# Kernel optimization log

Measured on AMD Instinct MI355X. Metric: run time of the kernel, lower is better.

## Reference

```python
import jax, jax.numpy as jnp
import numpy as np

B, N, IN_DIM, HID = 16, 2048, 128, 128
EPS = 1e-5


def _layer(x, W, b, g, beta):
    # x: (B, N, d_in) -> (B, N, HID)
    h = jnp.einsum('bnd,dh->bnh', x, W) + b
    mu = jnp.mean(h, axis=-1, keepdims=True)
    var = jnp.mean((h - mu) ** 2, axis=-1, keepdims=True)
    h = (h - mu) * jax.lax.rsqrt(var + EPS) * g + beta
    return jax.nn.relu(h)


def setup_inputs() -> dict:
    key = jax.random.key(0)
    ks = jax.random.split(key, 8)
    x = jax.random.normal(ks[0], (B, N, IN_DIM), dtype=jnp.float32)
    adj = jax.random.uniform(ks[1], (B, N, N), dtype=jnp.float32)
    inp = {'x': x, 'adj': adj}
    dims = [IN_DIM, HID, HID]
    for i in range(3):
        d_in = dims[i]
        scale = 1.0 / np.sqrt(d_in)
        inp[f'W{i}'] = jax.random.uniform(ks[2 + i], (d_in, HID), dtype=jnp.float32, minval=-scale, maxval=scale)
        inp[f'b{i}'] = jax.random.uniform(ks[5 + i], (HID,), dtype=jnp.float32, minval=-scale, maxval=scale)
        inp[f'g{i}'] = jnp.ones((HID,), dtype=jnp.float32)
        inp[f'be{i}'] = jnp.zeros((HID,), dtype=jnp.float32)
    return inp


def reference(x, adj, W0, b0, g0, be0, W1, b1, g1, be1, W2, b2, g2, be2):
    params = [(W0, b0, g0, be0), (W1, b1, g1, be1), (W2, b2, g2, be2)]
    h = x
    for (W, b, g, beta) in params:
        h_agg = jnp.einsum('bnm,bmd->bnd', adj, h)  # dense adjacency aggregation
        h = _layer(h_agg, W, b, g, beta)
    return h
```

## Files before the change

kernel.cpp:

```cpp
#include <hip/hip_runtime.h>
#include <hip/hip_bf16.h>

typedef __bf16 bf16;
typedef __bf16 bf16x8 __attribute__((ext_vector_type(8)));
typedef float  f32x4  __attribute__((ext_vector_type(4)));

static constexpr int NB  = 16;
static constexpr int NN  = 2048;
static constexpr int HID = 128;

__device__ __forceinline__ void gload_lds16(const bf16* g, bf16* l) {
    __builtin_amdgcn_global_load_lds(
        (const __attribute__((address_space(1))) unsigned int*)g,
        (__attribute__((address_space(3))) unsigned int*)l, 16, 0, 0);
}

#define WAITV(n) asm volatile("s_waitcnt vmcnt(" #n ")" ::: "memory")


__global__ __launch_bounds__(256) void prep_wt(const float* __restrict__ W0,
                                               const float* __restrict__ W1,
                                               const float* __restrict__ W2,
                                               bf16* __restrict__ WTg) {
    int l = blockIdx.x;
    const float* W = (l == 0) ? W0 : (l == 1) ? W1 : W2;
    bf16* out = WTg + l * 16384;
    int tid = threadIdx.x;
#pragma unroll
    for (int i = 0; i < 8; ++i) {
        int p = i * 256 + tid;
        int n = p >> 4, half = (p >> 3) & 1, cs = p & 7;
        int kc = cs ^ (n & 7);
        int kbase = half * 64 + kc * 8;
        bf16x8 o;
#pragma unroll
        for (int r = 0; r < 8; ++r) o[r] = (bf16)W[(kbase + r) * 128 + n];
        *(bf16x8*)(out + p * 8) = o;
    }
}

__global__ __launch_bounds__(256) void prep_xt(const float* __restrict__ x,
                                               bf16* __restrict__ xTt) {
    __shared__ bf16 T[128 * 136];
    const int blk = blockIdx.x;
    const int b = blk >> 4, node0 = (blk & 15) * 128;
    const int tid = threadIdx.x;
    const float* xb = x + ((size_t)b * NN + node0) * HID;
#pragma unroll
    for (int i = 0; i < 64; ++i) {
        int idx = i * 256 + tid;
        int node = idx >> 7, hid = idx & 127;
        T[hid * 136 + node] = (bf16)xb[(size_t)node * HID + hid];
    }
    __syncthreads();
#pragma unroll
    for (int i = 0; i < 8; ++i) {
        int p = i * 256 + tid;
        int half = p >> 10, p1 = p & 1023;
        int n = p1 >> 3, cs = p1 & 7, c = cs ^ (n & 7), m = half * 64 + c * 8;
        *(bf16x8*)(xTt + ((size_t)b * 32 + (node0 >> 6) + half) * 8192 + p1 * 8)
            = *(const bf16x8*)(T + n * 136 + m);
    }
}

template<int AMODE, bool FINAL>
__global__ __launch_bounds__(512, 2) void fused_layer(
        const float* __restrict__ Af, bf16* __restrict__ adjT,
        const bf16* __restrict__ Bt, const bf16* __restrict__ WTg,
        const float* __restrict__ bias, const float* __restrict__ gam,
        const float* __restrict__ bet, bf16* __restrict__ hOut,
        float* __restrict__ outF) {
    __shared__ __align__(16) bf16 lds[65536];

    const int tid = threadIdx.x, wave = tid >> 6, lane = tid & 63;
    const int c0 = lane & 15, q = lane >> 4;
    const int blk = blockIdx.x, xcd = blk & 7, jj = blk >> 3;
    const int b = xcd * 2 + (jj & 1);
    const int mtile = jj >> 1, m0 = mtile * 128;
    const int wm = wave >> 1, wn = wave & 1;

    const bf16* Btb = Bt + (size_t)b * 32 * 8192;
    bf16* Atl = adjT + ((size_t)b * 16 + mtile) * (size_t)32 * 8192;

    f32x4 acc[2][4] = {};

    auto stageA2 = [&](int buf, int kk) {
#pragma unroll
        for (int j = 0; j < 2; ++j) {
            int cb = j * 512 + wave * 64;
            gload_lds16(Atl + (size_t)kk * 8192 + (size_t)(cb + lane) * 8,
                        lds + buf * 16384 + cb * 8);
        }
    };
    auto stageB2 = [&](int buf, int kk) {
#pragma unroll
        for (int j = 0; j < 2; ++j) {
            int cb = j * 512 + wave * 64;
            gload_lds16(Btb + (size_t)kk * 8192 + (size_t)(cb + lane) * 8,
                        lds + buf * 16384 + 8192 + cb * 8);
        }
    };
    auto compute = [&](int buf) {
        const bf16* As = lds + buf * 16384;
        const bf16* Bs = As + 8192;
#pragma unroll
        for (int ks = 0; ks < 2; ++ks) {
            bf16x8 af[2], bf_[4];
#pragma unroll
            for (int mt = 0; mt < 2; ++mt) {
                int row = wm * 32 + mt * 16 + c0;
                int cb = (ks * 4 + q) ^ (row & 7);
                af[mt] = *(const bf16x8*)(As + row * 64 + cb * 8);
            }
#pragma unroll
            for (int nt = 0; nt < 4; ++nt) {
                int row = wn * 64 + nt * 16 + c0;
                int cb = (ks * 4 + q) ^ (row & 7);
                bf_[nt] = *(const bf16x8*)(Bs + row * 64 + cb * 8);
            }
            __builtin_amdgcn_s_setprio(1);
#pragma unroll
            for (int mt = 0; mt < 2; ++mt)
#pragma unroll
                for (int nt = 0; nt < 4; ++nt)
                    acc[mt][nt] = __builtin_amdgcn_mfma_f32_16x16x32_bf16(
                        af[mt], bf_[nt], acc[mt][nt], 0, 0, 0);
            __builtin_amdgcn_s_setprio(0);
        }
    };

    if constexpr (AMODE == 1) {
        int grow[2], gcb[2];
#pragma unroll
        for (int j = 0; j < 2; ++j) {
            int gi = j * 512 + tid;
            grow[j] = gi >> 3; gcb[j] = gi & 7;
        }
        f32x4 va[2], vb[2];
        auto loadA = [&](int kk) {
#pragma unroll
            for (int j = 0; j < 2; ++j) {
                const float* s = Af + (size_t)b * NN * NN
                               + (size_t)(m0 + grow[j]) * NN + kk * 64 + gcb[j] * 8;
                va[j] = *(const f32x4*)s;
                vb[j] = *(const f32x4*)(s + 4);
            }
        };
        auto writeA = [&](int buf, int kk) {
#pragma unroll
            for (int j = 0; j < 2; ++j) {
                bf16x8 o = {(bf16)va[j].x, (bf16)va[j].y, (bf16)va[j].z, (bf16)va[j].w,
                            (bf16)vb[j].x, (bf16)vb[j].y, (bf16)vb[j].z, (bf16)vb[j].w};
                int ch = grow[j] * 8 + (gcb[j] ^ (grow[j] & 7));
                *(bf16x8*)(lds + buf * 16384 + ch * 8) = o;
                *(bf16x8*)(Atl + (size_t)kk * 8192 + ch * 8) = o;
            }
        };
        loadA(0); stageB2(0, 0); writeA(0, 0);
        __syncthreads();
        int cur = 0;
        for (int kk = 0; kk < 32; ++kk) {
            if (kk < 31) { loadA(kk + 1); stageB2(cur ^ 1, kk + 1); }
            compute(cur);
            if (kk < 31) writeA(cur ^ 1, kk + 1);
            __syncthreads();
            cur ^= 1;
        }
    } else {
        stageA2(0, 0); stageB2(0, 0);
        stageA2(1, 1); stageB2(1, 1);
        stageA2(2, 2); stageB2(2, 2);
#pragma unroll 1
        for (int kk = 0; kk < 32; ++kk) {
            if (kk <= 29)      WAITV(8);
            else if (kk == 30) WAITV(4);
            else               WAITV(0);
            __builtin_amdgcn_s_barrier();
            asm volatile("" ::: "memory");
            compute(kk & 3);
            asm volatile("" ::: "memory");
            if (kk <= 28) { stageA2((kk + 3) & 3, kk + 3); stageB2((kk + 3) & 3, kk + 3); }
        }
        __syncthreads();
    }

    bf16* G = lds;
#pragma unroll
    for (int mt = 0; mt < 2; ++mt)
#pragma unroll
        for (int r = 0; r < 4; ++r) {
            int row = wm * 32 + mt * 16 + q * 4 + r;
#pragma unroll
            for (int nt = 0; nt < 4; ++nt) {
                int col = wn * 64 + nt * 16 + c0;
                G[row * 136 + col] = (bf16)acc[mt][nt][r];
            }
        }
    __syncthreads();

    f32x4 a2[8] = {};
    {
        const int gr = wave * 16 + c0;
#pragma unroll
        for (int ks = 0; ks < 4; ++ks) {
            bf16x8 af = *(const bf16x8*)(G + gr * 136 + ks * 32 + q * 8);
#pragma unroll
            for (int nt = 0; nt < 8; ++nt) {
                int n = nt * 16 + c0;
                int ch = n * 16 + (ks >> 1) * 8 + ((((ks & 1) << 2) | q) ^ (n & 7));
                bf16x8 bw = *(const bf16x8*)(WTg + (size_t)ch * 8);
                a2[nt] = __builtin_amdgcn_mfma_f32_16x16x32_bf16(af, bw, a2[nt], 0, 0, 0);
            }
        }
    }

    float bv[8], gv[8], ev[8];
#pragma unroll
    for (int nt = 0; nt < 8; ++nt) {
        int n = nt * 16 + c0;
        bv[nt] = bias[n]; gv[nt] = gam[n]; ev[nt] = bet[n];
    }
    bf16* Cs = lds;
    if constexpr (!FINAL) __syncthreads();
#pragma unroll
    for (int r = 0; r < 4; ++r) {
        float v[8], s1 = 0.f, s2 = 0.f;
#pragma unroll
        for (int nt = 0; nt < 8; ++nt) {
            float xv = a2[nt][r] + bv[nt];
            v[nt] = xv; s1 += xv; s2 += xv * xv;
        }
#pragma unroll
        for (int off = 1; off < 16; off <<= 1) {
            s1 += __shfl_xor(s1, off);
            s2 += __shfl_xor(s2, off);
        }
        float mu = s1 * (1.f / 128.f);
        float var = s2 * (1.f / 128.f) - mu * mu;
        float rs = rsqrtf(var + 1e-5f);
        int row = wave * 16 + q * 4 + r;
        if constexpr (FINAL) {
            size_t ro = ((size_t)b * NN + m0 + row) * HID;
#pragma unroll
            for (int nt = 0; nt < 8; ++nt) {
                float o = fmaxf((v[nt] - mu) * rs * gv[nt] + ev[nt], 0.f);
                outF[ro + nt * 16 + c0] = o;
            }
        } else {
#pragma unroll
            for (int nt = 0; nt < 8; ++nt) {
                float o = fmaxf((v[nt] - mu) * rs * gv[nt] + ev[nt], 0.f);
                Cs[(nt * 16 + c0) * 136 + row] = (bf16)o;
            }
        }
    }
    if constexpr (!FINAL) {
        __syncthreads();
#pragma unroll
        for (int i = 0; i < 4; ++i) {
            int p = i * 512 + tid;
            int half = p >> 10, p1 = p & 1023;
            int n = p1 >> 3, cs = p1 & 7, c = cs ^ (n & 7), m = half * 64 + c * 8;
            *(bf16x8*)(hOut + ((size_t)b * 32 + mtile * 2 + half) * 8192 + p1 * 8)
                = *(const bf16x8*)(Cs + n * 136 + m);
        }
    }
}

extern "C" void kernel_launch(void* const* d_in, const int* in_sizes, int n_in,
                              void* d_out, int out_size, void* d_ws, size_t ws_size,
                              hipStream_t stream) {
    const float* x   = (const float*)d_in[0];
    const float* adj = (const float*)d_in[1];
    const float* W[3]  = {(const float*)d_in[2],  (const float*)d_in[6],  (const float*)d_in[10]};
    const float* bb[3] = {(const float*)d_in[3],  (const float*)d_in[7],  (const float*)d_in[11]};
    const float* gg[3] = {(const float*)d_in[4],  (const float*)d_in[8],  (const float*)d_in[12]};
    const float* be[3] = {(const float*)d_in[5],  (const float*)d_in[9],  (const float*)d_in[13]};

    char* ws = (char*)d_ws;
    size_t off = 0;
    auto alloc = [&](size_t bytes) {
        char* p = ws + off; off = (off + bytes + 255) & ~(size_t)255; return p;
    };
    bf16* WTg  = (bf16*)alloc((size_t)3 * 16384 * 2);
    bf16* xTt  = (bf16*)alloc((size_t)NB * 32 * 8192 * 2);
    bf16* hT0  = (bf16*)alloc((size_t)NB * 32 * 8192 * 2);
    bf16* hT1  = (bf16*)alloc((size_t)NB * 32 * 8192 * 2);
    bf16* adjT = (bf16*)alloc((size_t)NB * 16 * 32 * 8192 * 2);

    float* outF = (float*)d_out;

    prep_wt<<<3, 256, 0, stream>>>(W[0], W[1], W[2], WTg);
    prep_xt<<<256, 256, 0, stream>>>(x, xTt);

    fused_layer<1, false><<<256, 512, 0, stream>>>(adj, adjT, xTt, WTg,
                                                   bb[0], gg[0], be[0], hT0, nullptr);
    fused_layer<2, false><<<256, 512, 0, stream>>>(adj, adjT, hT0, WTg + 16384,
                                                   bb[1], gg[1], be[1], hT1, nullptr);
    fused_layer<2, true ><<<256, 512, 0, stream>>>(adj, adjT, hT1, WTg + 2 * 16384,
                                                   bb[2], gg[2], be[2], nullptr, outF);
}
```

Before: 503.6 us.

## Split layer kernels: preload W into LDS for layer0, interleave prefetch in later layers

Splits the templated fused layer into a dedicated layer0 kernel and a layer8p kernel for the bf16-adjacency layers. Layer0 now loads the transposed weight matrix into a separate LDS region at kernel start, drops setprio, and shrinks its LDS footprint. Layer8p breaks each k-step's global-to-LDS prefetch into halves interleaved with MFMA sub-steps, separated by extra barriers, and lowers the occupancy hint to one block per CU. The goal is to spread memory issue across compute and overlap it better with MFMA, at the cost of more barriers and possibly lower occupancy.

```diff
diff --git a/kernel.cpp b/kernel.cpp
--- a/kernel.cpp
+++ b/kernel.cpp
@@ -63,14 +63,13 @@
     }
 }
 
-template<int AMODE, bool FINAL>
-__global__ __launch_bounds__(512, 2) void fused_layer(
+__global__ __launch_bounds__(512, 2) void layer0(
         const float* __restrict__ Af, bf16* __restrict__ adjT,
         const bf16* __restrict__ Bt, const bf16* __restrict__ WTg,
         const float* __restrict__ bias, const float* __restrict__ gam,
-        const float* __restrict__ bet, bf16* __restrict__ hOut,
-        float* __restrict__ outF) {
-    __shared__ __align__(16) bf16 lds[65536];
+        const float* __restrict__ bet, bf16* __restrict__ hOut) {
+    __shared__ __align__(16) bf16 lds[49152];
+    bf16* WTl = lds + 32768;
 
     const int tid = threadIdx.x, wave = tid >> 6, lane = tid & 63;
     const int c0 = lane & 15, q = lane >> 4;
@@ -84,14 +83,12 @@
 
     f32x4 acc[2][4] = {};
 
-    auto stageA2 = [&](int buf, int kk) {
-#pragma unroll
-        for (int j = 0; j < 2; ++j) {
-            int cb = j * 512 + wave * 64;
-            gload_lds16(Atl + (size_t)kk * 8192 + (size_t)(cb + lane) * 8,
-                        lds + buf * 16384 + cb * 8);
-        }
-    };
+#pragma unroll
+    for (int j = 0; j < 4; ++j) {
+        int cb = j * 512 + wave * 64;
+        gload_lds16(WTg + (size_t)(cb + lane) * 8, WTl + cb * 8);
+    }
+
     auto stageB2 = [&](int buf, int kk) {
 #pragma unroll
         for (int j = 0; j < 2; ++j) {
@@ -118,71 +115,207 @@
                 int cb = (ks * 4 + q) ^ (row & 7);
                 bf_[nt] = *(const bf16x8*)(Bs + row * 64 + cb * 8);
             }
-            __builtin_amdgcn_s_setprio(1);
 #pragma unroll
             for (int mt = 0; mt < 2; ++mt)
 #pragma unroll
                 for (int nt = 0; nt < 4; ++nt)
                     acc[mt][nt] = __builtin_amdgcn_mfma_f32_16x16x32_bf16(
                         af[mt], bf_[nt], acc[mt][nt], 0, 0, 0);
-            __builtin_amdgcn_s_setprio(0);
-        }
-    };
-
-    if constexpr (AMODE == 1) {
-        int grow[2], gcb[2];
+        }
+    };
+
+    int grow[2], gcb[2];
+#pragma unroll
+    for (int j = 0; j < 2; ++j) {
+        int gi = j * 512 + tid;
+        grow[j] = gi >> 3; gcb[j] = gi & 7;
+    }
+    f32x4 va[2], vb[2];
+    auto loadA = [&](int kk) {
 #pragma unroll
         for (int j = 0; j < 2; ++j) {
-            int gi = j * 512 + tid;
-            grow[j] = gi >> 3; gcb[j] = gi & 7;
-        }
-        f32x4 va[2], vb[2];
-        auto loadA = [&](int kk) {
-#pragma unroll
-            for (int j = 0; j < 2; ++j) {
-                const float* s = Af + (size_t)b * NN * NN
-                               + (size_t)(m0 + grow[j]) * NN + kk * 64 + gcb[j] * 8;
-                va[j] = *(const f32x4*)s;
-                vb[j] = *(const f32x4*)(s + 4);
-            }
-        };
-        auto writeA = [&](int buf, int kk) {
-#pragma unroll
-            for (int j = 0; j < 2; ++j) {
-                bf16x8 o = {(bf16)va[j].x, (bf16)va[j].y, (bf16)va[j].z, (bf16)va[j].w,
-                            (bf16)vb[j].x, (bf16)vb[j].y, (bf16)vb[j].z, (bf16)vb[j].w};
-                int ch = grow[j] * 8 + (gcb[j] ^ (grow[j] & 7));
-                *(bf16x8*)(lds + buf * 16384 + ch * 8) = o;
-                *(bf16x8*)(Atl + (size_t)kk * 8192 + ch * 8) = o;
-            }
-        };
-        loadA(0); stageB2(0, 0); writeA(0, 0);
+            const float* s = Af + (size_t)b * NN * NN
+                           + (size_t)(m0 + grow[j]) * NN + kk * 64 + gcb[j] * 8;
+            va[j] = *(const f32x4*)s;
+            vb[j] = *(const f32x4*)(s + 4);
+        }
+    };
+    auto writeA = [&](int buf, int kk) {
+#pragma unroll
+        for (int j = 0; j < 2; ++j) {
+            bf16x8 o = {(bf16)va[j].x, (bf16)va[j].y, (bf16)va[j].z, (bf16)va[j].w,
+                        (bf16)vb[j].x, (bf16)vb[j].y, (bf16)vb[j].z, (bf16)vb[j].w};
+            int ch = grow[j] * 8 + (gcb[j] ^ (grow[j] & 7));
+            *(bf16x8*)(lds + buf * 16384 + ch * 8) = o;
+            *(bf16x8*)(Atl + (size_t)kk * 8192 + ch * 8) = o;
+        }
+    };
+    loadA(0); stageB2(0, 0); writeA(0, 0);
+    __syncthreads();
+    int cur = 0;
+    for (int kk = 0; kk < 32; ++kk) {
+        if (kk < 31) { loadA(kk + 1); stageB2(cur ^ 1, kk + 1); }
+        compute(cur);
+        if (kk < 31) writeA(cur ^ 1, kk + 1);
         __syncthreads();
-        int cur = 0;
-        for (int kk = 0; kk < 32; ++kk) {
-            if (kk < 31) { loadA(kk + 1); stageB2(cur ^ 1, kk + 1); }
-            compute(cur);
-            if (kk < 31) writeA(cur ^ 1, kk + 1);
-            __syncthreads();
-            cur ^= 1;
-        }
-    } else {
-        stageA2(0, 0); stageB2(0, 0);
-        stageA2(1, 1); stageB2(1, 1);
-        stageA2(2, 2); stageB2(2, 2);
+        cur ^= 1;
+    }
+
+    bf16* G = lds;
+#pragma unroll
+    for (int mt = 0; mt < 2; ++mt)
+#pragma unroll
+        for (int r = 0; r < 4; ++r) {
+            int row = wm * 32 + mt * 16 + q * 4 + r;
+#pragma unroll
+            for (int nt = 0; nt < 4; ++nt) {
+                int col = wn * 64 + nt * 16 + c0;
+                G[row * 136 + col] = (bf16)acc[mt][nt][r];
+            }
+        }
+    __syncthreads();
+
+    f32x4 a2[8] = {};
+    {
+        const int gr = wave * 16 + c0;
+#pragma unroll
+        for (int ks = 0; ks < 4; ++ks) {
+            bf16x8 af = *(const bf16x8*)(G + gr * 136 + ks * 32 + q * 8);
+#pragma unroll
+            for (int nt = 0; nt < 8; ++nt) {
+                int n = nt * 16 + c0;
+                int ch = n * 16 + (ks >> 1) * 8 + ((((ks & 1) << 2) | q) ^ (n & 7));
+                bf16x8 bw = *(const bf16x8*)(WTl + ch * 8);
+                a2[nt] = __builtin_amdgcn_mfma_f32_16x16x32_bf16(af, bw, a2[nt], 0, 0, 0);
+            }
+        }
+    }
+
+    float bv[8], gv[8], ev[8];
+#pragma unroll
+    for (int nt = 0; nt < 8; ++nt) {
+        int n = nt * 16 + c0;
+        bv[nt] = bias[n]; gv[nt] = gam[n]; ev[nt] = bet[n];
+    }
+    bf16* Cs = lds;
+    __syncthreads();
+#pragma unroll
+    for (int r = 0; r < 4; ++r) {
+        float v[8], s1 = 0.f, s2 = 0.f;
+#pragma unroll
+        for (int nt = 0; nt < 8; ++nt) {
+            float xv = a2[nt][r] + bv[nt];
+            v[nt] = xv; s1 += xv; s2 += xv * xv;
+        }
+#pragma unroll
+        for (int off = 1; off < 16; off <<= 1) {
+            s1 += __shfl_xor(s1, off);
+            s2 += __shfl_xor(s2, off);
+        }
+        float mu = s1 * (1.f / 128.f);
+        float var = s2 * (1.f / 128.f) - mu * mu;
+        float rs = rsqrtf(var + 1e-5f);
+        int row = wave * 16 + q * 4 + r;
+#pragma unroll
+        for (int nt = 0; nt < 8; ++nt) {
+            float o = fmaxf((v[nt] - mu) * rs * gv[nt] + ev[nt], 0.f);
+            Cs[(nt * 16 + c0) * 136 + row] = (bf16)o;
+        }
+    }
+    __syncthreads();
+#pragma unroll
+    for (int i = 0; i < 4; ++i) {
+        int p = i * 512 + tid;
+        int half = p >> 10, p1 = p & 1023;
+        int n = p1 >> 3, cs = p1 & 7, c = cs ^ (n & 7), m = half * 64 + c * 8;
+        *(bf16x8*)(hOut + ((size_t)b * 32 + mtile * 2 + half) * 8192 + p1 * 8)
+            = *(const bf16x8*)(Cs + n * 136 + m);
+    }
+}
+
+template<bool FINAL>
+__global__ __launch_bounds__(512, 1) void layer8p(
+        bf16* __restrict__ adjT, const bf16* __restrict__ Bt,
+        const bf16* __restrict__ WTg,
+        const float* __restrict__ bias, const float* __restrict__ gam,
+        const float* __restrict__ bet, bf16* __restrict__ hOut,
+        float* __restrict__ outF) {
+    __shared__ __align__(16) bf16 lds[65536];
+
+    const int tid = threadIdx.x, wave = tid >> 6, lane = tid & 63;
+    const int c0 = lane & 15, q = lane >> 4;
+    const int blk = blockIdx.x, xcd = blk & 7, jj = blk >> 3;
+    const int b = xcd * 2 + (jj & 1);
+    const int mtile = jj >> 1, m0 = mtile * 128;
+    const int wm = wave >> 1, wn = wave & 1;
+
+    const bf16* Btb = Bt + (size_t)b * 32 * 8192;
+    bf16* Atl = adjT + ((size_t)b * 16 + mtile) * (size_t)32 * 8192;
+
+    f32x4 acc[2][4] = {};
+
+    auto gA = [&](int p, int kk, int buf) {
+        int cb = p * 512 + wave * 64;
+        gload_lds16(Atl + (size_t)kk * 8192 + (size_t)(cb + lane) * 8,
+                    lds + buf * 16384 + cb * 8);
+    };
+    auto gB = [&](int p, int kk, int buf) {
+        int cb = p * 512 + wave * 64;
+        gload_lds16(Btb + (size_t)kk * 8192 + (size_t)(cb + lane) * 8,
+                    lds + buf * 16384 + 8192 + cb * 8);
+    };
+
+#pragma unroll
+    for (int t = 0; t < 3; ++t) { gA(0, t, t); gA(1, t, t); gB(0, t, t); gB(1, t, t); }
+
 #pragma unroll 1
-        for (int kk = 0; kk < 32; ++kk) {
-            if (kk <= 29)      WAITV(8);
-            else if (kk == 30) WAITV(4);
-            else               WAITV(0);
-            __builtin_amdgcn_s_barrier();
-            asm volatile("" ::: "memory");
-            compute(kk & 3);
-            asm volatile("" ::: "memory");
-            if (kk <= 28) { stageA2((kk + 3) & 3, kk + 3); stageB2((kk + 3) & 3, kk + 3); }
-        }
-        __syncthreads();
-    }
+    for (int kk = 0; kk < 32; ++kk) {
+        const int buf = kk & 3, nb = (kk + 3) & 3;
+        const bool pf = (kk < 29);
+        if (kk <= 29)      WAITV(8);
+        else if (kk == 30) WAITV(4);
+        else               WAITV(0);
+        __builtin_amdgcn_s_barrier();
+        asm volatile("" ::: "memory");
+        const bf16* As = lds + buf * 16384;
+        const bf16* Bs = As + 8192;
+#pragma unroll
+        for (int ks = 0; ks < 2; ++ks) {
+            bf16x8 af[2];
+#pragma unroll
+            for (int mt = 0; mt < 2; ++mt) {
+                int row = wm * 32 + mt * 16 + c0;
+                int cb = (ks * 4 + q) ^ (row & 7);
+                af[mt] = *(const bf16x8*)(As + row * 64 + cb * 8);
+            }
+#pragma unroll
+            for (int half = 0; half < 2; ++half) {
+                if (pf) {
+                    if (ks == 0) gA(half, kk + 3, nb);
+                    else         gB(half, kk + 3, nb);
+                }
+                __builtin_amdgcn_s_barrier();
+                bf16x8 bf_[2];
+#pragma unroll
+                for (int j = 0; j < 2; ++j) {
+                    int nt = half * 2 + j;
+                    int row = wn * 64 + nt * 16 + c0;
+                    int cb = (ks * 4 + q) ^ (row & 7);
+                    bf_[j] = *(const bf16x8*)(Bs + row * 64 + cb * 8);
+                }
+                __builtin_amdgcn_s_setprio(1);
+#pragma unroll
+                for (int mt = 0; mt < 2; ++mt)
+#pragma unroll
+                    for (int j = 0; j < 2; ++j)
+                        acc[mt][half * 2 + j] = __builtin_amdgcn_mfma_f32_16x16x32_bf16(
+                            af[mt], bf_[j], acc[mt][half * 2 + j], 0, 0, 0);
+                __builtin_amdgcn_s_setprio(0);
+            }
+        }
+        asm volatile("" ::: "memory");
+    }
+    __syncthreads();
 
     bf16* G = lds;
 #pragma unroll
@@ -293,10 +426,10 @@
     prep_wt<<<3, 256, 0, stream>>>(W[0], W[1], W[2], WTg);
     prep_xt<<<256, 256, 0, stream>>>(x, xTt);
 
-    fused_layer<1, false><<<256, 512, 0, stream>>>(adj, adjT, xTt, WTg,
-                                                   bb[0], gg[0], be[0], hT0, nullptr);
-    fused_layer<2, false><<<256, 512, 0, stream>>>(adj, adjT, hT0, WTg + 16384,
-                                                   bb[1], gg[1], be[1], hT1, nullptr);
-    fused_layer<2, true ><<<256, 512, 0, stream>>>(adj, adjT, hT1, WTg + 2 * 16384,
-                                                   bb[2], gg[2], be[2], nullptr, outF);
-}
+    layer0<<<256, 512, 0, stream>>>(adj, adjT, xTt, WTg,
+                                    bb[0], gg[0], be[0], hT0);
+    layer8p<false><<<256, 512, 0, stream>>>(adjT, hT0, WTg + 16384,
+                                            bb[1], gg[1], be[1], hT1, nullptr);
+    layer8p<true ><<<256, 512, 0, stream>>>(adjT, hT1, WTg + 2 * 16384,
+                                            bb[2], gg[2], be[2], nullptr, outF);
+}
```

After: 501.1 us. Within noise of the previous version (-0.5%).

## Double K-tile per stage and replace 4-deep async pipeline with double buffering

Applied to the files above, without the earlier changes.

The aggregation loop now processes two 64-wide K tiles per stage (16 iterations instead of 32). Layers 1-2 drop the 4-stage vmcnt-managed ring buffer for a simple double buffer with full syncthreads. The setprio hints are removed, launch bounds change to one block per CU, and the epilogue is factored into a shared helper. Halving the barrier count should cut synchronisation overhead, at the cost of shallower prefetch depth and lower occupancy.

```diff
diff --git a/kernel.cpp b/kernel.cpp
--- a/kernel.cpp
+++ b/kernel.cpp
@@ -14,8 +14,6 @@
         (const __attribute__((address_space(1))) unsigned int*)g,
         (__attribute__((address_space(3))) unsigned int*)l, 16, 0, 0);
 }
-
-#define WAITV(n) asm volatile("s_waitcnt vmcnt(" #n ")" ::: "memory")
 
 
 __global__ __launch_bounds__(256) void prep_wt(const float* __restrict__ W0,
@@ -63,13 +61,105 @@
     }
 }
 
-template<int AMODE, bool FINAL>
-__global__ __launch_bounds__(512, 2) void fused_layer(
+template<bool FINAL>
+__device__ __forceinline__ void epilogue(
+        bf16* lds, const f32x4 (&acc)[2][4],
+        const bf16* __restrict__ WTg,
+        const float* __restrict__ bias, const float* __restrict__ gam,
+        const float* __restrict__ bet, bf16* __restrict__ hOut,
+        float* __restrict__ outF, int b, int mtile, int m0) {
+    const int tid = threadIdx.x, wave = tid >> 6, lane = tid & 63;
+    const int c0 = lane & 15, q = lane >> 4;
+    const int wm = wave >> 1, wn = wave & 1;
+
+    bf16* G = lds;
+#pragma unroll
+    for (int mt = 0; mt < 2; ++mt)
+#pragma unroll
+        for (int r = 0; r < 4; ++r) {
+            int row = wm * 32 + mt * 16 + q * 4 + r;
+#pragma unroll
+            for (int nt = 0; nt < 4; ++nt) {
+                int col = wn * 64 + nt * 16 + c0;
+                G[row * 136 + col] = (bf16)acc[mt][nt][r];
+            }
+        }
+    __syncthreads();
+
+    f32x4 a2[8] = {};
+    {
+        const int gr = wave * 16 + c0;
+#pragma unroll
+        for (int ks = 0; ks < 4; ++ks) {
+            bf16x8 af = *(const bf16x8*)(G + gr * 136 + ks * 32 + q * 8);
+#pragma unroll
+            for (int nt = 0; nt < 8; ++nt) {
+                int n = nt * 16 + c0;
+                int ch = n * 16 + (ks >> 1) * 8 + ((((ks & 1) << 2) | q) ^ (n & 7));
+                bf16x8 bw = *(const bf16x8*)(WTg + (size_t)ch * 8);
+                a2[nt] = __builtin_amdgcn_mfma_f32_16x16x32_bf16(af, bw, a2[nt], 0, 0, 0);
+            }
+        }
+    }
+
+    float bv[8], gv[8], ev[8];
+#pragma unroll
+    for (int nt = 0; nt < 8; ++nt) {
+        int n = nt * 16 + c0;
+        bv[nt] = bias[n]; gv[nt] = gam[n]; ev[nt] = bet[n];
+    }
+    bf16* Cs = lds;
+    if constexpr (!FINAL) __syncthreads();
+#pragma unroll
+    for (int r = 0; r < 4; ++r) {
+        float v[8], s1 = 0.f, s2 = 0.f;
+#pragma unroll
+        for (int nt = 0; nt < 8; ++nt) {
+            float xv = a2[nt][r] + bv[nt];
+            v[nt] = xv; s1 += xv; s2 += xv * xv;
+        }
+#pragma unroll
+        for (int off = 1; off < 16; off <<= 1) {
+            s1 += __shfl_xor(s1, off);
+            s2 += __shfl_xor(s2, off);
+        }
+        float mu = s1 * (1.f / 128.f);
+        float var = s2 * (1.f / 128.f) - mu * mu;
+        float rs = rsqrtf(var + 1e-5f);
+        int row = wave * 16 + q * 4 + r;
+        if constexpr (FINAL) {
+            size_t ro = ((size_t)b * NN + m0 + row) * HID;
+#pragma unroll
+            for (int nt = 0; nt < 8; ++nt) {
+                float o = fmaxf((v[nt] - mu) * rs * gv[nt] + ev[nt], 0.f);
+                outF[ro + nt * 16 + c0] = o;
+            }
+        } else {
+#pragma unroll
+            for (int nt = 0; nt < 8; ++nt) {
+                float o = fmaxf((v[nt] - mu) * rs * gv[nt] + ev[nt], 0.f);
+                Cs[(nt * 16 + c0) * 136 + row] = (bf16)o;
+            }
+        }
+    }
+    if constexpr (!FINAL) {
+        __syncthreads();
+#pragma unroll
+        for (int i = 0; i < 4; ++i) {
+            int p = i * 512 + tid;
+            int half = p >> 10, p1 = p & 1023;
+            int n = p1 >> 3, cs = p1 & 7, c = cs ^ (n & 7), m = half * 64 + c * 8;
+            *(bf16x8*)(hOut + ((size_t)b * 32 + mtile * 2 + half) * 8192 + p1 * 8)
+                = *(const bf16x8*)(Cs + n * 136 + m);
+        }
+    }
+}
+
+__global__ __launch_bounds__(512, 1) void layer0(
         const float* __restrict__ Af, bf16* __restrict__ adjT,
         const bf16* __restrict__ Bt, const bf16* __restrict__ WTg,
         const float* __restrict__ bias, const float* __restrict__ gam,
-        const float* __restrict__ bet, bf16* __restrict__ hOut,
-        float* __restrict__ outF) {
+        const float* __restrict__ bet, bf16* __restrict__ hOut) {
     __shared__ __align__(16) bf16 lds[65536];
 
     const int tid = threadIdx.x, wave = tid >> 6, lane = tid & 63;
@@ -84,187 +174,162 @@
 
     f32x4 acc[2][4] = {};
 
-    auto stageA2 = [&](int buf, int kk) {
-#pragma unroll
-        for (int j = 0; j < 2; ++j) {
+    auto stageB = [&](int buf, int t) {
+#pragma unroll
+        for (int j = 0; j < 4; ++j) {
             int cb = j * 512 + wave * 64;
-            gload_lds16(Atl + (size_t)kk * 8192 + (size_t)(cb + lane) * 8,
-                        lds + buf * 16384 + cb * 8);
-        }
-    };
-    auto stageB2 = [&](int buf, int kk) {
-#pragma unroll
-        for (int j = 0; j < 2; ++j) {
+            gload_lds16(Btb + (size_t)t * 16384 + (size_t)(cb + lane) * 8,
+                        lds + buf * 32768 + 16384 + cb * 8);
+        }
+    };
+    auto compute = [&](int buf) {
+        const bf16* As = lds + buf * 32768;
+        const bf16* Bs = As + 16384;
+#pragma unroll
+        for (int T = 0; T < 2; ++T)
+#pragma unroll
+            for (int ks = 0; ks < 2; ++ks) {
+                bf16x8 af[2], bf_[4];
+#pragma unroll
+                for (int mt = 0; mt < 2; ++mt) {
+                    int row = wm * 32 + mt * 16 + c0;
+                    int cb = (ks * 4 + q) ^ (row & 7);
+                    af[mt] = *(const bf16x8*)(As + T * 8192 + row * 64 + cb * 8);
+                }
+#pragma unroll
+                for (int nt = 0; nt < 4; ++nt) {
+                    int row = wn * 64 + nt * 16 + c0;
+                    int cb = (ks * 4 + q) ^ (row & 7);
+                    bf_[nt] = *(const bf16x8*)(Bs + T * 8192 + row * 64 + cb * 8);
+                }
+#pragma unroll
+                for (int mt = 0; mt < 2; ++mt)
+#pragma unroll
+                    for (int nt = 0; nt < 4; ++nt)
+                        acc[mt][nt] = __builtin_amdgcn_mfma_f32_16x16x32_bf16(
+                            af[mt], bf_[nt], acc[mt][nt], 0, 0, 0);
+            }
+    };
+
+    int g_row[4], g_cc[4];
+#pragma unroll
+    for (int j = 0; j < 4; ++j) {
+        int gi = j * 512 + tid;
+        g_row[j] = gi >> 4; g_cc[j] = gi & 15;
+    }
+    f32x4 va[4], vb[4];
+    auto loadA = [&](int t) {
+#pragma unroll
+        for (int j = 0; j < 4; ++j) {
+            const float* s = Af + (size_t)b * NN * NN
+                           + (size_t)(m0 + g_row[j]) * NN + t * 128 + g_cc[j] * 8;
+            va[j] = *(const f32x4*)s;
+            vb[j] = *(const f32x4*)(s + 4);
+        }
+    };
+    auto writeA = [&](int buf, int t) {
+#pragma unroll
+        for (int j = 0; j < 4; ++j) {
+            bf16x8 o = {(bf16)va[j].x, (bf16)va[j].y, (bf16)va[j].z, (bf16)va[j].w,
+                        (bf16)vb[j].x, (bf16)vb[j].y, (bf16)vb[j].z, (bf16)vb[j].w};
+            int tile = g_cc[j] >> 3, kc = g_cc[j] & 7;
+            int ch = g_row[j] * 8 + (kc ^ (g_row[j] & 7));
+            *(bf16x8*)(lds + buf * 32768 + tile * 8192 + ch * 8) = o;
+            *(bf16x8*)(Atl + (size_t)t * 16384 + (size_t)tile * 8192 + ch * 8) = o;
+        }
+    };
+
+    loadA(0); stageB(0, 0); writeA(0, 0);
+    __syncthreads();
+    int cur = 0;
+    for (int t = 0; t < 16; ++t) {
+        if (t < 15) { loadA(t + 1); stageB(cur ^ 1, t + 1); }
+        compute(cur);
+        if (t < 15) writeA(cur ^ 1, t + 1);
+        __syncthreads();
+        cur ^= 1;
+    }
+
+    epilogue<false>(lds, acc, WTg, bias, gam, bet, hOut, nullptr, b, mtile, m0);
+}
+
+template<bool FINAL>
+__global__ __launch_bounds__(512, 1) void layerK(
+        const bf16* __restrict__ adjT, const bf16* __restrict__ Bt,
+        const bf16* __restrict__ WTg,
+        const float* __restrict__ bias, const float* __restrict__ gam,
+        const float* __restrict__ bet, bf16* __restrict__ hOut,
+        float* __restrict__ outF) {
+    __shared__ __align__(16) bf16 lds[65536];
+
+    const int tid = threadIdx.x, wave = tid >> 6, lane = tid & 63;
+    const int c0 = lane & 15, q = lane >> 4;
+    const int blk = blockIdx.x, xcd = blk & 7, jj = blk >> 3;
+    const int b = xcd * 2 + (jj & 1);
+    const int mtile = jj >> 1, m0 = mtile * 128;
+    const int wm = wave >> 1, wn = wave & 1;
+
+    const bf16* Btb = Bt + (size_t)b * 32 * 8192;
+    const bf16* Atl = adjT + ((size_t)b * 16 + mtile) * (size_t)32 * 8192;
+
+    f32x4 acc[2][4] = {};
+
+    auto stageA = [&](int buf, int t) {
+#pragma unroll
+        for (int j = 0; j < 4; ++j) {
             int cb = j * 512 + wave * 64;
-            gload_lds16(Btb + (size_t)kk * 8192 + (size_t)(cb + lane) * 8,
-                        lds + buf * 16384 + 8192 + cb * 8);
+            gload_lds16(Atl + (size_t)t * 16384 + (size_t)(cb + lane) * 8,
+                        lds + buf * 32768 + cb * 8);
+        }
+    };
+    auto stageB = [&](int buf, int t) {
+#pragma unroll
+        for (int j = 0; j < 4; ++j) {
+            int cb = j * 512 + wave * 64;
+            gload_lds16(Btb + (size_t)t * 16384 + (size_t)(cb + lane) * 8,
+                        lds + buf * 32768 + 16384 + cb * 8);
         }
     };
     auto compute = [&](int buf) {
-        const bf16* As = lds + buf * 16384;
-        const bf16* Bs = As + 8192;
-#pragma unroll
-        for (int ks = 0; ks < 2; ++ks) {
-            bf16x8 af[2], bf_[4];
-#pragma unroll
-            for (int mt = 0; mt < 2; ++mt) {
-                int row = wm * 32 + mt * 16 + c0;
-                int cb = (ks * 4 + q) ^ (row & 7);
-                af[mt] = *(const bf16x8*)(As + row * 64 + cb * 8);
-            }
-#pragma unroll
-            for (int nt = 0; nt < 4; ++nt) {
-                int row = wn * 64 + nt * 16 + c0;
-                int cb = (ks * 4 + q) ^ (row & 7);
-                bf_[nt] = *(const bf16x8*)(Bs + row * 64 + cb * 8);
-            }
-            __builtin_amdgcn_s_setprio(1);
-#pragma unroll
-            for (int mt = 0; mt < 2; ++mt)
-#pragma unroll
-                for (int nt = 0; nt < 4; ++nt)
-                    acc[mt][nt] = __builtin_amdgcn_mfma_f32_16x16x32_bf16(
-                        af[mt], bf_[nt], acc[mt][nt], 0, 0, 0);
-            __builtin_amdgcn_s_setprio(0);
-        }
-    };
-
-    if constexpr (AMODE == 1) {
-        int grow[2], gcb[2];
-#pragma unroll
-        for (int j = 0; j < 2; ++j) {
-            int gi = j * 512 + tid;
-            grow[j] = gi >> 3; gcb[j] = gi & 7;
-        }
-        f32x4 va[2], vb[2];
-        auto loadA = [&](int kk) {
-#pragma unroll
-            for (int j = 0; j < 2; ++j) {
-                const float* s = Af + (size_t)b * NN * NN
-                               + (size_t)(m0 + grow[j]) * NN + kk * 64 + gcb[j] * 8;
-                va[j] = *(const f32x4*)s;
-                vb[j] = *(const f32x4*)(s + 4);
-            }
-        };
-        auto writeA = [&](int buf, int kk) {
-#pragma unroll
-            for (int j = 0; j < 2; ++j) {
-                bf16x8 o = {(bf16)va[j].x, (bf16)va[j].y, (bf16)va[j].z, (bf16)va[j].w,
-                            (bf16)vb[j].x, (bf16)vb[j].y, (bf16)vb[j].z, (bf16)vb[j].w};
-                int ch = grow[j] * 8 + (gcb[j] ^ (grow[j] & 7));
-                *(bf16x8*)(lds + buf * 16384 + ch * 8) = o;
-                *(bf16x8*)(Atl + (size_t)kk * 8192 + ch * 8) = o;
-            }
-        };
-        loadA(0); stageB2(0, 0); writeA(0, 0);
+        const bf16* As = lds + buf * 32768;
+        const bf16* Bs = As + 16384;
+#pragma unroll
+        for (int T = 0; T < 2; ++T)
+#pragma unroll
+            for (int ks = 0; ks < 2; ++ks) {
+                bf16x8 af[2], bf_[4];
+#pragma unroll
+                for (int mt = 0; mt < 2; ++mt) {
+                    int row = wm * 32 + mt * 16 + c0;
+                    int cb = (ks * 4 + q) ^ (row & 7);
+                    af[mt] = *(const bf16x8*)(As + T * 8192 + row * 64 + cb * 8);
+                }
+#pragma unroll
+                for (int nt = 0; nt < 4; ++nt) {
+                    int row = wn * 64 + nt * 16 + c0;
+                    int cb = (ks * 4 + q) ^ (row & 7);
+                    bf_[nt] = *(const bf16x8*)(Bs + T * 8192 + row * 64 + cb * 8);
+                }
+#pragma unroll
+                for (int mt = 0; mt < 2; ++mt)
+#pragma unroll
+                    for (int nt = 0; nt < 4; ++nt)
+                        acc[mt][nt] = __builtin_amdgcn_mfma_f32_16x16x32_bf16(
+                            af[mt], bf_[nt], acc[mt][nt], 0, 0, 0);
+            }
+    };
+
+    stageA(0, 0); stageB(0, 0);
+    __syncthreads();
+    int cur = 0;
+    for (int t = 0; t < 16; ++t) {
+        if (t < 15) { stageA(cur ^ 1, t + 1); stageB(cur ^ 1, t + 1); }
+        compute(cur);
         __syncthreads();
-        int cur = 0;
-        for (int kk = 0; kk < 32; ++kk) {
-            if (kk < 31) { loadA(kk + 1); stageB2(cur ^ 1, kk + 1); }
-            compute(cur);
-            if (kk < 31) writeA(cur ^ 1, kk + 1);
-            __syncthreads();
-            cur ^= 1;
-        }
-    } else {
-        stageA2(0, 0); stageB2(0, 0);
-        stageA2(1, 1); stageB2(1, 1);
-        stageA2(2, 2); stageB2(2, 2);
-#pragma unroll 1
-        for (int kk = 0; kk < 32; ++kk) {
-            if (kk <= 29)      WAITV(8);
-            else if (kk == 30) WAITV(4);
-            else               WAITV(0);
-            __builtin_amdgcn_s_barrier();
-            asm volatile("" ::: "memory");
-            compute(kk & 3);
-            asm volatile("" ::: "memory");
-            if (kk <= 28) { stageA2((kk + 3) & 3, kk + 3); stageB2((kk + 3) & 3, kk + 3); }
-        }
-        __syncthreads();
-    }
-
-    bf16* G = lds;
-#pragma unroll
-    for (int mt = 0; mt < 2; ++mt)
-#pragma unroll
-        for (int r = 0; r < 4; ++r) {
-            int row = wm * 32 + mt * 16 + q * 4 + r;
-#pragma unroll
-            for (int nt = 0; nt < 4; ++nt) {
-                int col = wn * 64 + nt * 16 + c0;
-                G[row * 136 + col] = (bf16)acc[mt][nt][r];
-            }
-        }
-    __syncthreads();
-
-    f32x4 a2[8] = {};
-    {
-        const int gr = wave * 16 + c0;
-#pragma unroll
-        for (int ks = 0; ks < 4; ++ks) {
-            bf16x8 af = *(const bf16x8*)(G + gr * 136 + ks * 32 + q * 8);
-#pragma unroll
-            for (int nt = 0; nt < 8; ++nt) {
-                int n = nt * 16 + c0;
-                int ch = n * 16 + (ks >> 1) * 8 + ((((ks & 1) << 2) | q) ^ (n & 7));
-                bf16x8 bw = *(const bf16x8*)(WTg + (size_t)ch * 8);
-                a2[nt] = __builtin_amdgcn_mfma_f32_16x16x32_bf16(af, bw, a2[nt], 0, 0, 0);
-            }
-        }
-    }
-
-    float bv[8], gv[8], ev[8];
-#pragma unroll
-    for (int nt = 0; nt < 8; ++nt) {
-        int n = nt * 16 + c0;
-        bv[nt] = bias[n]; gv[nt] = gam[n]; ev[nt] = bet[n];
-    }
-    bf16* Cs = lds;
-    if constexpr (!FINAL) __syncthreads();
-#pragma unroll
-    for (int r = 0; r < 4; ++r) {
-        float v[8], s1 = 0.f, s2 = 0.f;
-#pragma unroll
-        for (int nt = 0; nt < 8; ++nt) {
-            float xv = a2[nt][r] + bv[nt];
-            v[nt] = xv; s1 += xv; s2 += xv * xv;
-        }
-#pragma unroll
-        for (int off = 1; off < 16; off <<= 1) {
-            s1 += __shfl_xor(s1, off);
-            s2 += __shfl_xor(s2, off);
-        }
-        float mu = s1 * (1.f / 128.f);
-        float var = s2 * (1.f / 128.f) - mu * mu;
-        float rs = rsqrtf(var + 1e-5f);
-        int row = wave * 16 + q * 4 + r;
-        if constexpr (FINAL) {
-            size_t ro = ((size_t)b * NN + m0 + row) * HID;
-#pragma unroll
-            for (int nt = 0; nt < 8; ++nt) {
-                float o = fmaxf((v[nt] - mu) * rs * gv[nt] + ev[nt], 0.f);
-                outF[ro + nt * 16 + c0] = o;
-            }
-        } else {
-#pragma unroll
-            for (int nt = 0; nt < 8; ++nt) {
-                float o = fmaxf((v[nt] - mu) * rs * gv[nt] + ev[nt], 0.f);
-                Cs[(nt * 16 + c0) * 136 + row] = (bf16)o;
-            }
-        }
-    }
-    if constexpr (!FINAL) {
-        __syncthreads();
-#pragma unroll
-        for (int i = 0; i < 4; ++i) {
-            int p = i * 512 + tid;
-            int half = p >> 10, p1 = p & 1023;
-            int n = p1 >> 3, cs = p1 & 7, c = cs ^ (n & 7), m = half * 64 + c * 8;
-            *(bf16x8*)(hOut + ((size_t)b * 32 + mtile * 2 + half) * 8192 + p1 * 8)
-                = *(const bf16x8*)(Cs + n * 136 + m);
-        }
-    }
+        cur ^= 1;
+    }
+
+    epilogue<FINAL>(lds, acc, WTg, bias, gam, bet, hOut, outF, b, mtile, m0);
 }
 
 extern "C" void kernel_launch(void* const* d_in, const int* in_sizes, int n_in,
@@ -293,10 +358,10 @@
     prep_wt<<<3, 256, 0, stream>>>(W[0], W[1], W[2], WTg);
     prep_xt<<<256, 256, 0, stream>>>(x, xTt);
 
-    fused_layer<1, false><<<256, 512, 0, stream>>>(adj, adjT, xTt, WTg,
-                                                   bb[0], gg[0], be[0], hT0, nullptr);
-    fused_layer<2, false><<<256, 512, 0, stream>>>(adj, adjT, hT0, WTg + 16384,
-                                                   bb[1], gg[1], be[1], hT1, nullptr);
-    fused_layer<2, true ><<<256, 512, 0, stream>>>(adj, adjT, hT1, WTg + 2 * 16384,
-                                                   bb[2], gg[2], be[2], nullptr, outF);
-}
+    layer0<<<256, 512, 0, stream>>>(adj, adjT, xTt, WTg,
+                                    bb[0], gg[0], be[0], hT0);
+    layerK<false><<<256, 512, 0, stream>>>(adjT, hT0, WTg + 16384,
+                                           bb[1], gg[1], be[1], hT1, nullptr);
+    layerK<true ><<<256, 512, 0, stream>>>(adjT, hT1, WTg + 2 * 16384,
+                                           bb[2], gg[2], be[2], nullptr, outF);
+}
```

Measured after the change: 497.6 us. About the same (-1.2%).
